# Kernel tuning notes

Measured on AMD Instinct MI355X. Metric: run time of the kernel, lower is better.

The kernel has to match this reference:

```python
import jax, jax.numpy as jnp
import numpy as np

B, N, D = 4, 4096, 1024
H = 16
HD = D // H            # 64 head dim
M = 256                # num random features
LN_EPS = 1e-5
KERNEL_EPS = 1e-4


def _gaussian_orthogonal_matrix(rng, num_rows, num_cols):
    """FAVOR+ orthogonal random projection, scaling=0 (row-norm multipliers)."""
    blocks = []
    n_full = num_rows // num_cols
    for _ in range(n_full):
        g = rng.standard_normal((num_cols, num_cols))
        q, _ = np.linalg.qr(g)
        blocks.append(q.T)
    rem = num_rows - n_full * num_cols
    if rem > 0:
        g = rng.standard_normal((num_cols, num_cols))
        q, _ = np.linalg.qr(g)
        blocks.append(q.T[:rem])
    mat = np.concatenate(blocks, axis=0)
    # scaling == 0: multiplier = row norms of an unstructured gaussian matrix
    multiplier = np.linalg.norm(rng.standard_normal((num_rows, num_cols)), axis=1)
    return (multiplier[:, None] * mat).astype(np.float32)


def favor_features(data, proj, is_query):
    """Nonnegative softmax kernel features. data: [B,H,N,HD], proj: [M,HD]."""
    d = data.shape[-1]
    data_normalizer = d ** -0.25
    ratio = proj.shape[0] ** -0.5
    data_dash = jnp.einsum('bhnd,md->bhnm', data_normalizer * data, proj)
    diag = 0.5 * (data_normalizer ** 2) * jnp.sum(data * data, axis=-1, keepdims=True)
    if is_query:
        mx = jnp.max(data_dash, axis=-1, keepdims=True)
    else:
        mx = jnp.max(data_dash, axis=(-1, -2), keepdims=True)
    return ratio * (jnp.exp(data_dash - diag - mx) + KERNEL_EPS)


def layer_norm(x, g, b):
    mu = jnp.mean(x, axis=-1, keepdims=True)
    var = jnp.mean((x - mu) ** 2, axis=-1, keepdims=True)
    return (x - mu) * jax.lax.rsqrt(var + LN_EPS) * g + b


def setup_inputs() -> dict:
    key = jax.random.key(0)
    ks = jax.random.split(key, 16)
    s_d = (1.0 / np.sqrt(D)).astype('float32') if False else 1.0 / np.sqrt(D)
    def lin(k, fin, fout):
        kw, kb = jax.random.split(k)
        lim = 1.0 / np.sqrt(fin)
        w = jax.random.uniform(kw, (fin, fout), jnp.float32, -lim, lim)
        b = jax.random.uniform(kb, (fout,), jnp.float32, -lim, lim)
        return w, b
    wq, bq = lin(ks[0], D, D)
    wk, bk = lin(ks[1], D, D)
    wv, bv = lin(ks[2], D, D)
    wo, bo = lin(ks[3], D, D)
    w1, b1 = lin(ks[4], D, 4 * D)
    w2, b2 = lin(ks[5], 4 * D, D)
    proj = jnp.asarray(_gaussian_orthogonal_matrix(np.random.default_rng(0), M, HD))
    x = jax.random.normal(ks[6], (B, N, D), jnp.float32)
    return dict(
        x=x, wq=wq, bq=bq, wk=wk, bk=bk, wv=wv, bv=bv, wo=wo, bo=bo,
        proj=proj, w1=w1, b1=b1, w2=w2, b2=b2,
        ln1_g=jnp.ones((D,), jnp.float32), ln1_b=jnp.zeros((D,), jnp.float32),
        ln2_g=jnp.ones((D,), jnp.float32), ln2_b=jnp.zeros((D,), jnp.float32),
    )


def reference(x, wq, bq, wk, bk, wv, bv, wo, bo, proj, w1, b1, w2, b2,
              ln1_g, ln1_b, ln2_g, ln2_b):
    def split_heads(t):  # [B,N,D] -> [B,H,N,HD]
        return t.reshape(B, N, H, HD).transpose(0, 2, 1, 3)

    residual = x
    Q = split_heads(x @ wq + bq)
    K = split_heads(x @ wk + bk)
    V = split_heads(x @ wv + bv)

    Qp = favor_features(Q, proj, is_query=True)    # [B,H,N,M]
    Kp = favor_features(K, proj, is_query=False)   # [B,H,N,M]

    # linear attention: Q' (K'^T V), O(N*M*HD)
    kv = jnp.einsum('bhnm,bhnd->bhmd', Kp, V)
    attn = jnp.einsum('bhnm,bhmd->bhnd', Qp, kv)
    denom = jnp.einsum('bhnm,bhm->bhn', Qp, jnp.sum(Kp, axis=2))
    attn = attn / denom[..., None]

    attn = attn.transpose(0, 2, 1, 3).reshape(B, N, D)
    x = attn @ wo + bo
    x = layer_norm(x + residual, ln1_g, ln1_b)

    residual = x
    h = jax.nn.gelu(x @ w1 + b1, approximate=False)
    x = h @ w2 + b2
    x = layer_norm(x + residual, ln2_g, ln2_b)
    return x
```

## Files before the change

### kernel.cpp

```cpp
#include <hip/hip_runtime.h>
#include <math.h>

#define DEV __device__ __forceinline__

typedef __attribute__((ext_vector_type(8))) short frag8;
typedef __attribute__((ext_vector_type(4))) float facc4;
typedef __attribute__((ext_vector_type(4))) unsigned short us4;
typedef __attribute__((ext_vector_type(8))) unsigned short us8;

DEV float bf2f(unsigned short u){ union{unsigned i; float f;} x; x.i=((unsigned)u)<<16; return x.f; }
DEV unsigned short f2bf(float f){ union{float f; unsigned i;} x; x.f=f;
  return (unsigned short)((x.i + 0x7FFFu + ((x.i>>16)&1u))>>16); }

#define GLD16(g, l) __builtin_amdgcn_global_load_lds( \
    (const __attribute__((address_space(1))) void*)(g), \
    (__attribute__((address_space(3))) void*)(l), 16, 0, 0)

template<int ROWS>
DEV void stage_tile(const unsigned short* __restrict__ g0, int ld, unsigned short* s0){
  static_assert(ROWS % 8 == 0, "");
  constexpr int SLOTS = ROWS/8;
  const int w = threadIdx.x>>6, lane = threadIdx.x&63;
  for (int s = w; s < SLOTS; s += 4) {
    int c  = (s<<6) + lane;
    int r  = c >> 3, cg = c & 7;
    int kg = cg ^ (r & 7);
    GLD16(g0 + (size_t)r*ld + (kg<<3), s0 + (s<<9));
  }
}

DEV frag8 frag_ld(const unsigned short* s, int row, int kg){
  int cg = kg ^ (row & 7);
  return *(const frag8*)(s + (row<<6) + (cg<<3));
}

template<int BM, int BN, int WR, int WC>
DEV void gemm_core(const unsigned short* __restrict__ Ag, int lda,
                   const unsigned short* __restrict__ Bg, int ldb,
                   int kIters, unsigned short* As, unsigned short* Bs,
                   facc4 (&acc)[BM/(WR*16)][BN/(WC*16)]) {
  constexpr int WM = BM/(WR*16), WN = BN/(WC*16);
  const int tid = threadIdx.x, w = tid>>6, lane = tid&63;
  const int wr = w / WC, wc = w % WC;
  const int col = lane & 15, quad = lane >> 4;
  for (int kt = 0; kt < kIters; ++kt) {
    stage_tile<BM>(Ag + kt*64, lda, As);
    stage_tile<BN>(Bg + kt*64, ldb, Bs);
    __syncthreads();
    #pragma unroll
    for (int ks = 0; ks < 2; ++ks) {
      frag8 af[WM], bfr[WN];
      #pragma unroll
      for (int i=0;i<WM;++i) af[i]  = frag_ld(As, wr*WM*16 + i*16 + col, ks*4+quad);
      #pragma unroll
      for (int j=0;j<WN;++j) bfr[j] = frag_ld(Bs, wc*WN*16 + j*16 + col, ks*4+quad);
      #pragma unroll
      for (int i=0;i<WM;++i)
        #pragma unroll
        for (int j=0;j<WN;++j)
          acc[i][j] = __builtin_amdgcn_mfma_f32_16x16x32_bf16(af[i], bfr[j], acc[i][j], 0,0,0);
    }
    __syncthreads();
  }
}

#define ZERO_ACC(acc, I, J) { facc4 zz = {0.f,0.f,0.f,0.f}; \
  _Pragma("unroll") for(int i_=0;i_<I;++i_) _Pragma("unroll") for(int j_=0;j_<J;++j_) acc[i_][j_]=zz; }

DEV void tr64(const float* __restrict__ in, unsigned short* __restrict__ out, int K, int N){
  __shared__ float t[64][65];
  const int bx = blockIdx.x*64, by = blockIdx.y*64;
  const int tid = threadIdx.x;
  const int r0 = tid>>4, c4 = (tid&15)*4;
  #pragma unroll
  for(int it=0; it<4; ++it){
    int r = r0 + it*16;
    float4 v = *(const float4*)(in + (size_t)(by+r)*N + bx + c4);
    t[r][c4+0]=v.x; t[r][c4+1]=v.y; t[r][c4+2]=v.z; t[r][c4+3]=v.w;
  }
  __syncthreads();
  #pragma unroll
  for(int it=0; it<4; ++it){
    int n = r0 + it*16;
    us4 o;
    #pragma unroll
    for(int e=0;e<4;++e) o[e] = f2bf(t[c4+e][n]);
    *(us4*)(out + (size_t)(bx+n)*K + by + c4) = o;
  }
}

__global__ void k_transpose4(const float* __restrict__ wq, const float* __restrict__ wk,
                             const float* __restrict__ wv, const float* __restrict__ wo,
                             unsigned short* __restrict__ wqkvT, unsigned short* __restrict__ woT){
  const float* in; unsigned short* out;
  int z = blockIdx.z;
  if(z==0){in=wq; out=wqkvT;} else if(z==1){in=wk; out=wqkvT+1048576;}
  else if(z==2){in=wv; out=wqkvT+2097152;} else {in=wo; out=woT;}
  tr64(in, out, 1024, 1024);
}

__global__ void k_transpose(const float* __restrict__ in, unsigned short* __restrict__ out,
                            int K, int N){ tr64(in, out, K, N); }

__global__ void k_cvt4(const float* __restrict__ in, unsigned short* __restrict__ out, int n4){
  int i = blockIdx.x*256 + threadIdx.x;
  if(i<n4){ float4 v = ((const float4*)in)[i];
    us4 o = {f2bf(v.x),f2bf(v.y),f2bf(v.z),f2bf(v.w)};
    ((us4*)out)[i]=o; }
}

__global__ void k_vones(unsigned short* __restrict__ Vt){
  int i = blockIdx.x*256+threadIdx.x;
  int head=i>>12, n=i&4095;
  Vt[((size_t)head*80+64)*4096 + n] = 0x3F80;
}

__global__ __launch_bounds__(256,2) void k_qkv(const unsigned short* __restrict__ xb,
    const unsigned short* __restrict__ wqkvT,
    const float* __restrict__ bq, const float* __restrict__ bk, const float* __restrict__ bv,
    unsigned short* __restrict__ Qb, unsigned short* __restrict__ Kb, unsigned short* __restrict__ Vt){
  __shared__ __align__(16) unsigned short As[128*64];
  __shared__ __align__(16) unsigned short Bs[128*64];
  facc4 acc[4][4]; ZERO_ACC(acc,4,4)
  const int bm = blockIdx.x, bn = blockIdx.y;
  gemm_core<128,128,2,2>(xb + (size_t)bm*128*1024, 1024,
                         wqkvT + (size_t)bn*128*1024, 1024, 16, As, Bs, acc);
  const int tid=threadIdx.x, w=tid>>6, lane=tid&63, col=lane&15, quad=lane>>4;
  const int wr=w>>1, wc=w&1;
  #pragma unroll
  for(int i=0;i<4;++i){
    int row0 = bm*128 + wr*64 + i*16 + quad*4;
    int bb = row0 >> 12, n0 = row0 & 4095;
    #pragma unroll
    for(int j=0;j<4;++j){
      int c = bn*128 + wc*64 + j*16 + col;
      int region = c >> 10, f = c & 1023, he = f >> 6, hd = f & 63;
      const float* bias = (region==0)? bq : (region==1)? bk : bv;
      float bsv = bias[f];
      if(region < 2){
        unsigned short* dst = (region==0? Qb : Kb) + ((size_t)(bb*16+he)*4096 + n0)*64 + hd;
        #pragma unroll
        for(int r=0;r<4;++r) dst[(size_t)r*64] = f2bf(acc[i][j][r] + bsv);
      } else {
        us4 pk;
        #pragma unroll
        for(int r=0;r<4;++r) pk[r] = f2bf(acc[i][j][r] + bsv);
        *(us4*)(Vt + ((size_t)(bb*16+he)*80 + hd)*4096 + n0) = pk;
      }
    }
  }
}

__global__ __launch_bounds__(256,2) void k_featq(const unsigned short* __restrict__ Qb,
    const unsigned short* __restrict__ projB, unsigned short* __restrict__ Qp, int qbase){
  __shared__ __align__(16) unsigned short As[64*64];
  __shared__ __align__(16) unsigned short Bs[256*64];
  __shared__ float diagS[64];
  facc4 acc[1][16]; ZERO_ACC(acc,1,16)
  const int br = blockIdx.x;
  gemm_core<64,256,4,1>(Qb + ((size_t)(qbase*1024 + br))*4096, 64, projB, 64, 1, As, Bs, acc);
  if (threadIdx.x < 64){
    int t=threadIdx.x; float ss=0.f;
    #pragma unroll
    for(int kg=0;kg<8;++kg){ int cg=kg^(t&7); const unsigned short* p = As + t*64 + cg*8;
      #pragma unroll
      for(int e=0;e<8;++e){ float v=bf2f(p[e]); ss+=v*v; } }
    diagS[t]=0.0625f*ss;
  }
  __syncthreads();
  const int w=threadIdx.x>>6, lane=threadIdx.x&63, col=lane&15, quad=lane>>4;
  const float dn=0.35355339059327378f;
  float mx[4];
  #pragma unroll
  for(int r=0;r<4;++r){ float m=-1e30f;
    #pragma unroll
    for(int j=0;j<16;++j) m=fmaxf(m, acc[0][j][r]);
    #pragma unroll
    for(int d=1; d<16; d<<=1) m=fmaxf(m, __shfl_xor(m,d));
    mx[r]=m*dn;
  }
  size_t tok0 = (size_t)br*64;
  #pragma unroll
  for(int j=0;j<16;++j){
    #pragma unroll
    for(int r=0;r<4;++r){
      int t = w*16 + quad*4 + r;
      float dd = dn*acc[0][j][r];
      Qp[(tok0 + t)*256 + j*16 + col] = f2bf(0.0625f*(expf(dd - diagS[t] - mx[r]) + 1e-4f));
    }
  }
}

__global__ __launch_bounds__(256,2) void k_featk_max(const unsigned short* __restrict__ Kb,
    const unsigned short* __restrict__ projB, float* __restrict__ pmax){
  __shared__ __align__(16) unsigned short As[64*64];
  __shared__ __align__(16) unsigned short Bs[256*64];
  __shared__ float wm[4];
  facc4 acc[1][16]; ZERO_ACC(acc,1,16)
  const int br = blockIdx.x;
  gemm_core<64,256,4,1>(Kb + (size_t)br*64*64, 64, projB, 64, 1, As, Bs, acc);
  const int w=threadIdx.x>>6, lane=threadIdx.x&63;
  float m=-1e30f;
  #pragma unroll
  for(int j=0;j<16;++j)
    #pragma unroll
    for(int r=0;r<4;++r) m=fmaxf(m, acc[0][j][r]);
  #pragma unroll
  for(int d=1; d<64; d<<=1) m=fmaxf(m, __shfl_xor(m,d));
  if(lane==0) wm[w]=m;
  __syncthreads();
  if(threadIdx.x==0)
    pmax[br] = fmaxf(fmaxf(wm[0],wm[1]),fmaxf(wm[2],wm[3])) * 0.35355339059327378f;
}

__global__ void k_mxk(const float* __restrict__ pmax, float* __restrict__ mxK){
  int h = threadIdx.x;
  float m=-1e30f;
  for(int i=0;i<64;++i) m=fmaxf(m, pmax[h*64+i]);
  mxK[h]=m;
}

__global__ __launch_bounds__(256,2) void k_featk(const unsigned short* __restrict__ Kb,
    const unsigned short* __restrict__ projB, const float* __restrict__ mxK,
    unsigned short* __restrict__ KpT, int qbase){
  __shared__ __align__(16) unsigned short As[64*64];
  __shared__ __align__(16) unsigned short Bs[256*64];
  __shared__ float diagS[64];
  facc4 acc[1][16]; ZERO_ACC(acc,1,16)
  const int br = blockIdx.x;
  gemm_core<64,256,4,1>(Kb + ((size_t)(qbase*1024 + br))*4096, 64, projB, 64, 1, As, Bs, acc);
  if (threadIdx.x < 64){
    int t=threadIdx.x; float ss=0.f;
    #pragma unroll
    for(int kg=0;kg<8;++kg){ int cg=kg^(t&7); const unsigned short* p = As + t*64 + cg*8;
      #pragma unroll
      for(int e=0;e<8;++e){ float v=bf2f(p[e]); ss+=v*v; } }
    diagS[t]=0.0625f*ss;
  }
  __syncthreads();
  const int lh = br >> 6;
  const float mxh = mxK[qbase*16 + lh];
  const int w=threadIdx.x>>6, lane=threadIdx.x&63, col=lane&15, quad=lane>>4;
  const int n0 = (br&63)*64 + w*16 + quad*4;
  const float dn=0.35355339059327378f;
  #pragma unroll
  for(int j=0;j<16;++j){
    us4 pk;
    #pragma unroll
    for(int r=0;r<4;++r){
      int t = w*16 + quad*4 + r;
      float dd = dn*acc[0][j][r];
      pk[r] = f2bf(0.0625f*(expf(dd - diagS[t] - mxh) + 1e-4f));
    }
    *(us4*)(KpT + ((size_t)lh*256 + j*16 + col)*4096 + n0) = pk;
  }
}

__global__ __launch_bounds__(256,2) void k_kv(const unsigned short* __restrict__ KpT,
    const unsigned short* __restrict__ Vt, float* __restrict__ part, int qbase){
  __shared__ __align__(16) unsigned short As[256*64];
  __shared__ __align__(16) unsigned short Bs[80*64];
  facc4 acc[4][5]; ZERO_ACC(acc,4,5)
  const int ksp = blockIdx.x, lh = blockIdx.y;
  gemm_core<256,80,4,1>(KpT + (size_t)lh*1048576 + ksp*256, 4096,
                        Vt  + ((size_t)(qbase*16+lh))*327680 + ksp*256, 4096, 4, As, Bs, acc);
  const int w=threadIdx.x>>6, lane=threadIdx.x&63, col=lane&15, quad=lane>>4;
  #pragma unroll
  for(int i=0;i<4;++i){
    int mp0 = w*64 + i*16 + quad*4;
    #pragma unroll
    for(int j=0;j<5;++j){
      int d = j*16+col;
      *(facc4*)(part + (((size_t)(ksp*16 + lh))*80 + d)*256 + mp0) = acc[i][j];
    }
  }
}

__global__ void k_kvred(const float* __restrict__ part, unsigned short* __restrict__ kvT, int qbase){
  int i = blockIdx.x*256 + threadIdx.x;
  float s=0.f;
  #pragma unroll
  for(int ks=0;ks<16;++ks) s += part[(size_t)ks*327680 + i];
  kvT[(size_t)qbase*327680 + i] = f2bf(s);
}

__global__ __launch_bounds__(256,2) void k_attn(const unsigned short* __restrict__ Qp,
    const unsigned short* __restrict__ kvT, unsigned short* __restrict__ attnOut, int qbase){
  __shared__ __align__(16) unsigned short As[128*64];
  __shared__ __align__(16) unsigned short Bs[80*64];
  facc4 acc[2][5]; ZERO_ACC(acc,2,5)
  const int mb = blockIdx.x, lh = blockIdx.y;
  gemm_core<128,80,4,1>(Qp  + (size_t)lh*1048576 + (size_t)mb*32768, 256,
                        kvT + ((size_t)(qbase*16+lh))*20480, 256, 4, As, Bs, acc);
  const int w=threadIdx.x>>6, lane=threadIdx.x&63, col=lane&15, quad=lane>>4;
  const int gh = qbase*16 + lh, b = gh>>4, h = gh&15;
  #pragma unroll
  for(int i=0;i<2;++i){
    #pragma unroll
    for(int r=0;r<4;++r){
      float den = __shfl(acc[i][4][r], lane & 48);
      float inv = 1.0f/den;
      int n = mb*128 + w*32 + i*16 + quad*4 + r;
      size_t base = ((size_t)(b*4096 + n))*1024 + h*64;
      #pragma unroll
      for(int j=0;j<4;++j)
        attnOut[base + j*16 + col] = f2bf(acc[i][j][r]*inv);
    }
  }
}

__global__ __launch_bounds__(256,2) void k_oproj(const unsigned short* __restrict__ attnOut,
    const unsigned short* __restrict__ woT, const float* __restrict__ bo,
    const float* __restrict__ x, unsigned short* __restrict__ y1){
  __shared__ __align__(16) unsigned short As[128*64];
  __shared__ __align__(16) unsigned short Bs[128*64];
  facc4 acc[4][4]; ZERO_ACC(acc,4,4)
  const int bm = blockIdx.x, bn = blockIdx.y;
  gemm_core<128,128,2,2>(attnOut + (size_t)bm*128*1024, 1024,
                         woT + (size_t)bn*128*1024, 1024, 16, As, Bs, acc);
  const int tid=threadIdx.x, w=tid>>6, lane=tid&63, col=lane&15, quad=lane>>4;
  const int wr=w>>1, wc=w&1;
  #pragma unroll
  for(int i=0;i<4;++i){
    int row0 = bm*128 + wr*64 + i*16 + quad*4;
    #pragma unroll
    for(int j=0;j<4;++j){
      int c = bn*128 + wc*64 + j*16 + col;
      float bsv = bo[c];
      #pragma unroll
      for(int r=0;r<4;++r){
        size_t idx = (size_t)(row0+r)*1024 + c;
        y1[idx] = f2bf(acc[i][j][r] + bsv + x[idx]);
      }
    }
  }
}

__global__ __launch_bounds__(256,2) void k_ffn1(const unsigned short* __restrict__ xb2,
    const unsigned short* __restrict__ w1T, const float* __restrict__ b1,
    unsigned short* __restrict__ hbuf, int hbase){
  __shared__ __align__(16) unsigned short As[128*64];
  __shared__ __align__(16) unsigned short Bs[128*64];
  facc4 acc[4][4]; ZERO_ACC(acc,4,4)
  const int bm = blockIdx.x, bn = blockIdx.y;
  gemm_core<128,128,2,2>(xb2 + ((size_t)(hbase*64 + bm))*131072, 1024,
                         w1T + (size_t)bn*128*1024, 1024, 16, As, Bs, acc);
  const int tid=threadIdx.x, w=tid>>6, lane=tid&63, col=lane&15, quad=lane>>4;
  const int wr=w>>1, wc=w&1;
  #pragma unroll
  for(int i=0;i<4;++i){
    int lrow0 = bm*128 + wr*64 + i*16 + quad*4;
    #pragma unroll
    for(int j=0;j<4;++j){
      int c = bn*128 + wc*64 + j*16 + col;
      float bsv = b1[c];
      #pragma unroll
      for(int r=0;r<4;++r){
        float v = acc[i][j][r] + bsv;
        float g = 0.5f*v*(1.0f+erff(v*0.70710678118654752f));
        hbuf[(size_t)(lrow0+r)*4096 + c] = f2bf(g);
      }
    }
  }
}

__global__ __launch_bounds__(256,2) void k_ffn2(const unsigned short* __restrict__ hbuf,
    const unsigned short* __restrict__ w2T, const float* __restrict__ b2,
    const unsigned short* __restrict__ xb2, unsigned short* __restrict__ y2, int hbase){
  __shared__ __align__(16) unsigned short As[128*64];
  __shared__ __align__(16) unsigned short Bs[128*64];
  facc4 acc[4][4]; ZERO_ACC(acc,4,4)
  const int bm = blockIdx.x, bn = blockIdx.y;
  gemm_core<128,128,2,2>(hbuf + (size_t)bm*128*4096, 4096,
                         w2T + (size_t)bn*128*4096, 4096, 64, As, Bs, acc);
  const int tid=threadIdx.x, w=tid>>6, lane=tid&63, col=lane&15, quad=lane>>4;
  const int wr=w>>1, wc=w&1;
  #pragma unroll
  for(int i=0;i<4;++i){
    int grow0 = hbase*8192 + bm*128 + wr*64 + i*16 + quad*4;
    #pragma unroll
    for(int j=0;j<4;++j){
      int c = bn*128 + wc*64 + j*16 + col;
      float bsv = b2[c];
      #pragma unroll
      for(int r=0;r<4;++r){
        size_t idx = (size_t)(grow0+r)*1024 + c;
        y2[idx] = f2bf(acc[i][j][r] + bsv + bf2f(xb2[idx]));
      }
    }
  }
}

__global__ __launch_bounds__(256) void k_lnb(const unsigned short* __restrict__ in,
    const float* __restrict__ g, const float* __restrict__ b,
    float* __restrict__ outf, unsigned short* __restrict__ outb){
  const int row = blockIdx.x*4 + (threadIdx.x>>6);
  const int lane = threadIdx.x&63;
  const unsigned short* x = in + (size_t)row*1024 + lane*16;
  float v[16];
  float s=0.f, s2=0.f;
  #pragma unroll
  for(int q=0;q<2;++q){ us8 u = *(const us8*)(x + q*8);
    #pragma unroll
    for(int e=0;e<8;++e){ float f=bf2f(u[e]); v[q*8+e]=f; s+=f; s2+=f*f; } }
  #pragma unroll
  for(int d=32;d;d>>=1){ s+=__shfl_xor(s,d); s2+=__shfl_xor(s2,d); }
  float mu = s*(1.0f/1024.0f), var = s2*(1.0f/1024.0f)-mu*mu;
  float rinv = rsqrtf(var+1e-5f);
  const int cb = lane*16;
  if(outf){
    #pragma unroll
    for(int q=0;q<4;++q){
      float4 o;
      o.x=(v[q*4+0]-mu)*rinv*g[cb+q*4+0]+b[cb+q*4+0];
      o.y=(v[q*4+1]-mu)*rinv*g[cb+q*4+1]+b[cb+q*4+1];
      o.z=(v[q*4+2]-mu)*rinv*g[cb+q*4+2]+b[cb+q*4+2];
      o.w=(v[q*4+3]-mu)*rinv*g[cb+q*4+3]+b[cb+q*4+3];
      *(float4*)(outf + (size_t)row*1024 + cb + q*4) = o;
    }
  }
  if(outb){
    #pragma unroll
    for(int q=0;q<2;++q){
      us8 o;
      #pragma unroll
      for(int e=0;e<8;++e) o[e]=f2bf((v[q*8+e]-mu)*rinv*g[cb+q*8+e]+b[cb+q*8+e]);
      *(us8*)(outb + (size_t)row*1024 + cb + q*8) = o;
    }
  }
}

extern "C" void kernel_launch(void* const* d_in, const int* in_sizes, int n_in,
                              void* d_out, int out_size, void* d_ws, size_t ws_size,
                              hipStream_t stream){
  const float* x   = (const float*)d_in[0];
  const float* wq  = (const float*)d_in[1];
  const float* bq  = (const float*)d_in[2];
  const float* wk  = (const float*)d_in[3];
  const float* bk  = (const float*)d_in[4];
  const float* wv  = (const float*)d_in[5];
  const float* bv  = (const float*)d_in[6];
  const float* wo  = (const float*)d_in[7];
  const float* bo  = (const float*)d_in[8];
  const float* proj= (const float*)d_in[9];
  const float* w1  = (const float*)d_in[10];
  const float* b1  = (const float*)d_in[11];
  const float* w2  = (const float*)d_in[12];
  const float* b2  = (const float*)d_in[13];
  const float* ln1g= (const float*)d_in[14];
  const float* ln1b= (const float*)d_in[15];
  const float* ln2g= (const float*)d_in[16];
  const float* ln2b= (const float*)d_in[17];
  (void)in_sizes; (void)n_in; (void)out_size;

  char* ws = (char*)d_ws;
  size_t off = 0;
  auto alloc = [&](size_t bytes)->char*{ char* p = ws + off; off += (bytes + 255) & ~(size_t)255; return p; };
  unsigned short* wqkvT = (unsigned short*)alloc(6291456);
  unsigned short* woT   = (unsigned short*)alloc(2097152);
  unsigned short* w1T   = (unsigned short*)alloc(8388608);
  unsigned short* w2T   = (unsigned short*)alloc(8388608);
  unsigned short* projB = (unsigned short*)alloc(32768);
  unsigned short* kvT   = (unsigned short*)alloc(2621440);
  float* pmax = (float*)alloc(16384);
  float* mxK  = (float*)alloc(256);
  char* R = alloc(230686720ull);
  if (off > ws_size) return;

  unsigned short* xb   = (unsigned short*)R;
  unsigned short* Qp   = (unsigned short*)R;
  unsigned short* y1   = (unsigned short*)R;
  unsigned short* Qb   = (unsigned short*)(R + 33554432);
  unsigned short* xb2  = (unsigned short*)(R + 33554432);
  unsigned short* Kb   = (unsigned short*)(R + 67108864);
  unsigned short* hbuf = (unsigned short*)(R + 67108864);
  unsigned short* Vt   = (unsigned short*)(R + 100663296);
  unsigned short* KpT  = (unsigned short*)(R + 142606336);
  float*          kvpart = (float*)(R + 176160768);
  unsigned short* attnOut = (unsigned short*)(R + 197132288);
  unsigned short* y2   = (unsigned short*)(R + 197132288);

  dim3 blk(256);
  k_transpose4<<<dim3(16,16,4),blk,0,stream>>>(wq, wk, wv, wo, wqkvT, woT);
  k_transpose<<<dim3(64,16),blk,0,stream>>>(w1, w1T, 1024, 4096);
  k_transpose<<<dim3(16,64),blk,0,stream>>>(w2, w2T, 4096, 1024);
  k_cvt4<<<16384,blk,0,stream>>>(x, xb, 4194304);
  k_cvt4<<<16,blk,0,stream>>>(proj, projB, 4096);
  k_vones<<<1024,blk,0,stream>>>(Vt);

  k_qkv<<<dim3(128,24),blk,0,stream>>>(xb, wqkvT, bq, bk, bv, Qb, Kb, Vt);
  k_featk_max<<<4096,blk,0,stream>>>(Kb, projB, pmax);
  k_mxk<<<1,64,0,stream>>>(pmax, mxK);

  for (int q = 0; q < 4; ++q) {
    k_featq<<<1024,blk,0,stream>>>(Qb, projB, Qp, q);
    k_featk<<<1024,blk,0,stream>>>(Kb, projB, mxK, KpT, q);
    k_kv<<<dim3(16,16),blk,0,stream>>>(KpT, Vt, kvpart, q);
    k_kvred<<<1280,blk,0,stream>>>(kvpart, kvT, q);
    k_attn<<<dim3(32,16),blk,0,stream>>>(Qp, kvT, attnOut, q);
  }

  k_oproj<<<dim3(128,8),blk,0,stream>>>(attnOut, woT, bo, x, y1);
  k_lnb<<<4096,blk,0,stream>>>(y1, ln1g, ln1b, nullptr, xb2);

  for (int h = 0; h < 2; ++h) {
    k_ffn1<<<dim3(64,32),blk,0,stream>>>(xb2, w1T, b1, hbuf, h);
    k_ffn2<<<dim3(64,8),blk,0,stream>>>(hbuf, w2T, b2, xb2, y2, h);
  }
  k_lnb<<<4096,blk,0,stream>>>(y2, ln2g, ln2b, (float*)d_out, nullptr);
}
```

Baseline: 1.054 ms.

## Enlarge feature-map tiles, stage outputs through LDS, vectorize reductions, merge prep kernels

Merges the x/proj conversion and V-ones init into one launch. Doubles the token tile of the FAVOR feature kernels to 128 with a 2x2 warp layout and writes Qp/KpT through a swizzled LDS staging buffer, so global stores become 16-byte coalesced. The attention output is staged the same way. kvred is vectorized to float4. The aim is to cut scattered narrow global stores and launch count, at the cost of extra LDS round trips and syncs, and possibly lower occupancy from the larger tiles.

```diff
diff --git a/kernel.cpp b/kernel.cpp
--- a/kernel.cpp
+++ b/kernel.cpp
@@ -102,17 +102,25 @@
 __global__ void k_transpose(const float* __restrict__ in, unsigned short* __restrict__ out,
                             int K, int N){ tr64(in, out, K, N); }
 
-__global__ void k_cvt4(const float* __restrict__ in, unsigned short* __restrict__ out, int n4){
-  int i = blockIdx.x*256 + threadIdx.x;
-  if(i<n4){ float4 v = ((const float4*)in)[i];
+__global__ void k_misc(const float* __restrict__ x, unsigned short* __restrict__ xb,
+                       const float* __restrict__ proj, unsigned short* __restrict__ projB,
+                       unsigned short* __restrict__ Vt){
+  int bx = blockIdx.x, tid = threadIdx.x;
+  if(bx < 16384){
+    int i = bx*256 + tid;
+    float4 v = ((const float4*)x)[i];
     us4 o = {f2bf(v.x),f2bf(v.y),f2bf(v.z),f2bf(v.w)};
-    ((us4*)out)[i]=o; }
-}
-
-__global__ void k_vones(unsigned short* __restrict__ Vt){
-  int i = blockIdx.x*256+threadIdx.x;
-  int head=i>>12, n=i&4095;
-  Vt[((size_t)head*80+64)*4096 + n] = 0x3F80;
+    ((us4*)xb)[i]=o;
+  } else if(bx < 16400){
+    int i = (bx-16384)*256 + tid;
+    if(i<4096){ float4 v = ((const float4*)proj)[i];
+      us4 o = {f2bf(v.x),f2bf(v.y),f2bf(v.z),f2bf(v.w)};
+      ((us4*)projB)[i]=o; }
+  } else {
+    int i = (bx-16400)*256 + tid;
+    int head=i>>12, n=i&4095;
+    Vt[((size_t)head*80+64)*4096 + n] = 0x3F80;
+  }
 }
 
 __global__ __launch_bounds__(256,2) void k_qkv(const unsigned short* __restrict__ xb,
@@ -153,58 +161,82 @@
 
 __global__ __launch_bounds__(256,2) void k_featq(const unsigned short* __restrict__ Qb,
     const unsigned short* __restrict__ projB, unsigned short* __restrict__ Qp, int qbase){
-  __shared__ __align__(16) unsigned short As[64*64];
+  __shared__ __align__(16) unsigned short As[128*64];
   __shared__ __align__(16) unsigned short Bs[256*64];
-  __shared__ float diagS[64];
-  facc4 acc[1][16]; ZERO_ACC(acc,1,16)
+  __shared__ float diagS[128];
+  __shared__ float maxS[128][2];
+  facc4 acc[4][8]; ZERO_ACC(acc,4,8)
   const int br = blockIdx.x;
-  gemm_core<64,256,4,1>(Qb + ((size_t)(qbase*1024 + br))*4096, 64, projB, 64, 1, As, Bs, acc);
-  if (threadIdx.x < 64){
-    int t=threadIdx.x; float ss=0.f;
-    #pragma unroll
-    for(int kg=0;kg<8;++kg){ int cg=kg^(t&7); const unsigned short* p = As + t*64 + cg*8;
-      #pragma unroll
-      for(int e=0;e<8;++e){ float v=bf2f(p[e]); ss+=v*v; } }
-    diagS[t]=0.0625f*ss;
-  }
+  gemm_core<128,256,2,2>(Qb + ((size_t)qbase*65536 + (size_t)br*128)*64, 64,
+                         projB, 64, 1, As, Bs, acc);
+  const int tid=threadIdx.x, w=tid>>6, lane=tid&63, col=lane&15, quad=lane>>4;
+  const int wr=w>>1, wc=w&1;
+  if(tid<128){ float ss=0.f;
+    #pragma unroll
+    for(int kg=0;kg<8;++kg){ frag8 v = frag_ld(As, tid, kg);
+      #pragma unroll
+      for(int e=0;e<8;++e){ float f=bf2f((unsigned short)v[e]); ss+=f*f; } }
+    diagS[tid]=0.0625f*ss; }
+  #pragma unroll
+  for(int i=0;i<4;++i)
+    #pragma unroll
+    for(int r=0;r<4;++r){
+      float m=-1e30f;
+      #pragma unroll
+      for(int j=0;j<8;++j) m=fmaxf(m,acc[i][j][r]);
+      #pragma unroll
+      for(int d=1;d<16;d<<=1) m=fmaxf(m,__shfl_xor(m,d));
+      if(col==0) maxS[wr*64+i*16+quad*4+r][wc]=m;
+    }
   __syncthreads();
-  const int w=threadIdx.x>>6, lane=threadIdx.x&63, col=lane&15, quad=lane>>4;
   const float dn=0.35355339059327378f;
-  float mx[4];
-  #pragma unroll
-  for(int r=0;r<4;++r){ float m=-1e30f;
-    #pragma unroll
-    for(int j=0;j<16;++j) m=fmaxf(m, acc[0][j][r]);
-    #pragma unroll
-    for(int d=1; d<16; d<<=1) m=fmaxf(m, __shfl_xor(m,d));
-    mx[r]=m*dn;
-  }
-  size_t tok0 = (size_t)br*64;
-  #pragma unroll
-  for(int j=0;j<16;++j){
-    #pragma unroll
-    for(int r=0;r<4;++r){
-      int t = w*16 + quad*4 + r;
-      float dd = dn*acc[0][j][r];
-      Qp[(tok0 + t)*256 + j*16 + col] = f2bf(0.0625f*(expf(dd - diagS[t] - mx[r]) + 1e-4f));
-    }
-  }
-}
-
-__global__ __launch_bounds__(256,2) void k_featk_max(const unsigned short* __restrict__ Kb,
+  unsigned short* Ct = Bs;
+  size_t tokbase = (size_t)br*128;
+  #pragma unroll
+  for(int p=0;p<2;++p){
+    if(wr==p){
+      #pragma unroll
+      for(int i=0;i<4;++i)
+        #pragma unroll
+        for(int r=0;r<4;++r){
+          int tl = i*16+quad*4+r;
+          int tf = p*64+tl;
+          float dsub = diagS[tf] + dn*fmaxf(maxS[tf][0],maxS[tf][1]);
+          #pragma unroll
+          for(int j=0;j<8;++j){
+            int m = wc*128 + j*16 + col;
+            float val = 0.0625f*(__expf(dn*acc[i][j][r] - dsub) + 1e-4f);
+            int cc = m>>3;
+            Ct[tl*256 + ((cc ^ (tl&31))<<3) + (m&7)] = f2bf(val);
+          }
+        }
+    }
+    __syncthreads();
+    for(int c=tid;c<2048;c+=256){
+      int tl=c>>5, part=c&31;
+      us8 v = *(const us8*)(Ct + tl*256 + ((part ^ (tl&31))<<3));
+      *(us8*)(Qp + (tokbase + p*64 + tl)*256 + part*8) = v;
+    }
+    __syncthreads();
+  }
+}
+
+__global__ __launch_bounds__(256,2) void k_fkmax(const unsigned short* __restrict__ Kb,
     const unsigned short* __restrict__ projB, float* __restrict__ pmax){
-  __shared__ __align__(16) unsigned short As[64*64];
+  __shared__ __align__(16) unsigned short As[128*64];
   __shared__ __align__(16) unsigned short Bs[256*64];
   __shared__ float wm[4];
-  facc4 acc[1][16]; ZERO_ACC(acc,1,16)
+  facc4 acc[4][8]; ZERO_ACC(acc,4,8)
   const int br = blockIdx.x;
-  gemm_core<64,256,4,1>(Kb + (size_t)br*64*64, 64, projB, 64, 1, As, Bs, acc);
+  gemm_core<128,256,2,2>(Kb + (size_t)br*8192, 64, projB, 64, 1, As, Bs, acc);
   const int w=threadIdx.x>>6, lane=threadIdx.x&63;
   float m=-1e30f;
   #pragma unroll
-  for(int j=0;j<16;++j)
-    #pragma unroll
-    for(int r=0;r<4;++r) m=fmaxf(m, acc[0][j][r]);
+  for(int i=0;i<4;++i)
+    #pragma unroll
+    for(int j=0;j<8;++j)
+      #pragma unroll
+      for(int r=0;r<4;++r) m=fmaxf(m, acc[i][j][r]);
   #pragma unroll
   for(int d=1; d<64; d<<=1) m=fmaxf(m, __shfl_xor(m,d));
   if(lane==0) wm[w]=m;
@@ -216,43 +248,58 @@
 __global__ void k_mxk(const float* __restrict__ pmax, float* __restrict__ mxK){
   int h = threadIdx.x;
   float m=-1e30f;
-  for(int i=0;i<64;++i) m=fmaxf(m, pmax[h*64+i]);
+  for(int i=0;i<32;++i) m=fmaxf(m, pmax[h*32+i]);
   mxK[h]=m;
 }
 
 __global__ __launch_bounds__(256,2) void k_featk(const unsigned short* __restrict__ Kb,
     const unsigned short* __restrict__ projB, const float* __restrict__ mxK,
     unsigned short* __restrict__ KpT, int qbase){
-  __shared__ __align__(16) unsigned short As[64*64];
+  __shared__ __align__(16) unsigned short As[128*64];
   __shared__ __align__(16) unsigned short Bs[256*64];
-  __shared__ float diagS[64];
-  facc4 acc[1][16]; ZERO_ACC(acc,1,16)
+  __shared__ float diagS[128];
+  facc4 acc[4][8]; ZERO_ACC(acc,4,8)
   const int br = blockIdx.x;
-  gemm_core<64,256,4,1>(Kb + ((size_t)(qbase*1024 + br))*4096, 64, projB, 64, 1, As, Bs, acc);
-  if (threadIdx.x < 64){
-    int t=threadIdx.x; float ss=0.f;
-    #pragma unroll
-    for(int kg=0;kg<8;++kg){ int cg=kg^(t&7); const unsigned short* p = As + t*64 + cg*8;
-      #pragma unroll
-      for(int e=0;e<8;++e){ float v=bf2f(p[e]); ss+=v*v; } }
-    diagS[t]=0.0625f*ss;
-  }
+  gemm_core<128,256,2,2>(Kb + ((size_t)qbase*65536 + (size_t)br*128)*64, 64,
+                         projB, 64, 1, As, Bs, acc);
+  const int tid=threadIdx.x, w=tid>>6, lane=tid&63, col=lane&15, quad=lane>>4;
+  const int wr=w>>1, wc=w&1;
+  if(tid<128){ float ss=0.f;
+    #pragma unroll
+    for(int kg=0;kg<8;++kg){ frag8 v = frag_ld(As, tid, kg);
+      #pragma unroll
+      for(int e=0;e<8;++e){ float f=bf2f((unsigned short)v[e]); ss+=f*f; } }
+    diagS[tid]=0.0625f*ss; }
   __syncthreads();
-  const int lh = br >> 6;
+  const int lh = br>>5, n0 = (br&31)*128;
   const float mxh = mxK[qbase*16 + lh];
-  const int w=threadIdx.x>>6, lane=threadIdx.x&63, col=lane&15, quad=lane>>4;
-  const int n0 = (br&63)*64 + w*16 + quad*4;
   const float dn=0.35355339059327378f;
-  #pragma unroll
-  for(int j=0;j<16;++j){
-    us4 pk;
-    #pragma unroll
-    for(int r=0;r<4;++r){
-      int t = w*16 + quad*4 + r;
-      float dd = dn*acc[0][j][r];
-      pk[r] = f2bf(0.0625f*(expf(dd - diagS[t] - mxh) + 1e-4f));
-    }
-    *(us4*)(KpT + ((size_t)lh*256 + j*16 + col)*4096 + n0) = pk;
+  unsigned short* Ct = Bs;
+  #pragma unroll
+  for(int p=0;p<2;++p){
+    if(wc==p){
+      #pragma unroll
+      for(int i=0;i<4;++i)
+        #pragma unroll
+        for(int r=0;r<4;++r){
+          int tok = wr*64 + i*16 + quad*4 + r;
+          float dsub = diagS[tok] + mxh;
+          int tc = tok>>3;
+          #pragma unroll
+          for(int j=0;j<8;++j){
+            int ml = j*16 + col;
+            float val = 0.0625f*(__expf(dn*acc[i][j][r] - dsub) + 1e-4f);
+            Ct[ml*128 + ((tc ^ (ml&15))<<3) + (tok&7)] = f2bf(val);
+          }
+        }
+    }
+    __syncthreads();
+    for(int c=tid;c<2048;c+=256){
+      int ml=c>>4, part=c&15;
+      us8 v = *(const us8*)(Ct + ml*128 + ((part ^ (ml&15))<<3));
+      *(us8*)(KpT + ((size_t)(lh*256 + p*128 + ml))*4096 + n0 + part*8) = v;
+    }
+    __syncthreads();
   }
 }
 
@@ -278,10 +325,12 @@
 
 __global__ void k_kvred(const float* __restrict__ part, unsigned short* __restrict__ kvT, int qbase){
   int i = blockIdx.x*256 + threadIdx.x;
-  float s=0.f;
-  #pragma unroll
-  for(int ks=0;ks<16;++ks) s += part[(size_t)ks*327680 + i];
-  kvT[(size_t)qbase*327680 + i] = f2bf(s);
+  float4 s = {0.f,0.f,0.f,0.f};
+  #pragma unroll
+  for(int ks=0;ks<16;++ks){ float4 v = ((const float4*)part)[(size_t)ks*81920 + i];
+    s.x+=v.x; s.y+=v.y; s.z+=v.z; s.w+=v.w; }
+  us4 o = {f2bf(s.x),f2bf(s.y),f2bf(s.z),f2bf(s.w)};
+  ((us4*)kvT)[(size_t)qbase*81920 + i] = o;
 }
 
 __global__ __launch_bounds__(256,2) void k_attn(const unsigned short* __restrict__ Qp,
@@ -294,18 +343,27 @@
                         kvT + ((size_t)(qbase*16+lh))*20480, 256, 4, As, Bs, acc);
   const int w=threadIdx.x>>6, lane=threadIdx.x&63, col=lane&15, quad=lane>>4;
   const int gh = qbase*16 + lh, b = gh>>4, h = gh&15;
-  #pragma unroll
-  for(int i=0;i<2;++i){
+  unsigned short* Ct = As;
+  #pragma unroll
+  for(int i=0;i<2;++i)
     #pragma unroll
     for(int r=0;r<4;++r){
       float den = __shfl(acc[i][4][r], lane & 48);
       float inv = 1.0f/den;
-      int n = mb*128 + w*32 + i*16 + quad*4 + r;
-      size_t base = ((size_t)(b*4096 + n))*1024 + h*64;
-      #pragma unroll
-      for(int j=0;j<4;++j)
-        attnOut[base + j*16 + col] = f2bf(acc[i][j][r]*inv);
-    }
+      int tok = w*32 + i*16 + quad*4 + r;
+      #pragma unroll
+      for(int j=0;j<4;++j){
+        int hd = j*16 + col;
+        int cc = hd>>3;
+        Ct[tok*64 + ((cc ^ (tok&7))<<3) + (hd&7)] = f2bf(acc[i][j][r]*inv);
+      }
+    }
+  __syncthreads();
+  const int n0 = mb*128;
+  for(int c=threadIdx.x;c<1024;c+=256){
+    int row=c>>3, part=c&7;
+    us8 v = *(const us8*)(Ct + row*64 + ((part ^ (row&7))<<3));
+    *(us8*)(attnOut + ((size_t)(b*4096) + n0 + row)*1024 + h*64 + part*8) = v;
   }
 }
 
@@ -469,7 +527,6 @@
 
   unsigned short* xb   = (unsigned short*)R;
   unsigned short* Qp   = (unsigned short*)R;
-  unsigned short* y1   = (unsigned short*)R;
   unsigned short* Qb   = (unsigned short*)(R + 33554432);
   unsigned short* xb2  = (unsigned short*)(R + 33554432);
   unsigned short* Kb   = (unsigned short*)(R + 67108864);
@@ -479,24 +536,23 @@
   float*          kvpart = (float*)(R + 176160768);
   unsigned short* attnOut = (unsigned short*)(R + 197132288);
   unsigned short* y2   = (unsigned short*)(R + 197132288);
+  unsigned short* y1   = (unsigned short*)R;
 
   dim3 blk(256);
   k_transpose4<<<dim3(16,16,4),blk,0,stream>>>(wq, wk, wv, wo, wqkvT, woT);
   k_transpose<<<dim3(64,16),blk,0,stream>>>(w1, w1T, 1024, 4096);
   k_transpose<<<dim3(16,64),blk,0,stream>>>(w2, w2T, 4096, 1024);
-  k_cvt4<<<16384,blk,0,stream>>>(x, xb, 4194304);
-  k_cvt4<<<16,blk,0,stream>>>(proj, projB, 4096);
-  k_vones<<<1024,blk,0,stream>>>(Vt);
+  k_misc<<<17424,blk,0,stream>>>(x, xb, proj, projB, Vt);
 
   k_qkv<<<dim3(128,24),blk,0,stream>>>(xb, wqkvT, bq, bk, bv, Qb, Kb, Vt);
-  k_featk_max<<<4096,blk,0,stream>>>(Kb, projB, pmax);
+  k_fkmax<<<2048,blk,0,stream>>>(Kb, projB, pmax);
   k_mxk<<<1,64,0,stream>>>(pmax, mxK);
 
   for (int q = 0; q < 4; ++q) {
-    k_featq<<<1024,blk,0,stream>>>(Qb, projB, Qp, q);
-    k_featk<<<1024,blk,0,stream>>>(Kb, projB, mxK, KpT, q);
+    k_featq<<<512,blk,0,stream>>>(Qb, projB, Qp, q);
+    k_featk<<<512,blk,0,stream>>>(Kb, projB, mxK, KpT, q);
     k_kv<<<dim3(16,16),blk,0,stream>>>(KpT, Vt, kvpart, q);
-    k_kvred<<<1280,blk,0,stream>>>(kvpart, kvT, q);
+    k_kvred<<<320,blk,0,stream>>>(kvpart, kvT, q);
     k_attn<<<dim3(32,16),blk,0,stream>>>(Qp, kvT, attnOut, q);
   }
 
```

Result: faster. 1.009 ms (-4.3%).
